# Performance work log

Measured on AMD Instinct MI355X. Metric: run time of the kernel, lower is better.

The kernel has to match this reference:

```python
import jax, jax.numpy as jnp
import numpy as np

ALPHA = 0.1
B, T, D = 32, 1024, 384


def _build_alive(T):
    # Expert j (1-indexed) is created at time j with lifetime 2^(ctz(j)+2)+1.
    def lifetime(j):
        k = (j & -j).bit_length() - 1
        return 2 ** (k + 2) + 1

    sets = [[j for j in range(1, t + 1) if t < j + lifetime(j)]
            for t in range(1, T + 1)]
    K = max(len(s) for s in sets)
    # pad with sentinel index T (the extra never-consumed expert slot)
    idx = np.full((T, K), T, dtype=np.int32)
    mask = np.zeros((T, K), dtype=np.float32)
    for t0, s in enumerate(sets):
        for i, j in enumerate(s):
            idx[t0, i] = j - 1  # 0-indexed expert slot
            mask[t0, i] = 1.0
    return idx, mask


def setup_inputs() -> dict:
    key = jax.random.key(0)
    kx, kw, kb = jax.random.split(key, 3)
    n_exp = T + 1
    x = jax.random.normal(kx, (B, T, D), dtype=jnp.float32)
    # stand-in STULayer = Linear(D, D) per expert
    W = jax.random.normal(kw, (n_exp, D, D), dtype=jnp.float32) / np.float32(np.sqrt(D))
    b = jax.random.normal(kb, (n_exp, D), dtype=jnp.float32) * 0.02
    idx, mask = _build_alive(T)
    return {"x": x, "W": W, "b": b,
            "alive_idx": jnp.asarray(idx), "alive_mask": jnp.asarray(mask)}


def reference(x, W, b, alive_idx, alive_mask):
    Bb, Tt, Dd = x.shape
    n_exp = W.shape[0]
    # initial pool: 1 expert with weight 1
    p0 = jnp.zeros((n_exp,), x.dtype).at[0].set(1.0)
    new_idx = jnp.arange(1, Tt + 1, dtype=jnp.int32)      # slot of expert created at step t
    t_f = jnp.arange(1, Tt + 1, dtype=x.dtype)            # p[new] = 1/t

    def step(p, inp):
        x_t, idx, mask, ni, tf = inp          # x_t: [B,D]; idx,mask: [K]
        Wg = W[idx]                            # [K,D,D]
        bg = b[idx]                            # [K,D]
        outs = jnp.einsum('bd,kde->kbe', x_t, Wg) + bg[:, None, :]  # [K,B,D]
        p_a = p[idx] * mask                    # weights of alive experts
        w = p_a / jnp.sum(p_a)                 # normalized (torch keeps them pre-normalized)
        y_t = jnp.einsum('k,kbe->be', w, outs)
        # soft cross-entropy of expert outputs against x_t (ChunkedCrossEntropyLoss stand-in)
        tgt = jax.nn.softmax(x_t, axis=-1)                       # [B,D]
        logp = jax.nn.log_softmax(outs, axis=-1)                 # [K,B,D]
        loss = -jnp.mean(jnp.sum(tgt[None, :, :] * logp, axis=-1), axis=-1)  # [K]
        loss = jax.lax.stop_gradient(loss)     # torch uses .item() => detached
        # multiplicative weight update, normalize over alive set
        p_upd = p_a * jnp.exp(-ALPHA * loss) * mask
        p_upd = p_upd / jnp.sum(p_upd)
        p = p.at[idx].set(jnp.where(mask > 0, p_upd, p[idx]))
        # spawn new expert with weight 1/t (renormalization deferred to use time)
        p = p.at[ni].set(1.0 / tf)
        return p, y_t

    xs = (jnp.swapaxes(x, 0, 1), alive_idx, alive_mask, new_idx, t_f)
    _, ys = jax.lax.scan(step, p0, xs)        # ys: [T,B,D]
    return jnp.swapaxes(ys, 0, 1)
```

## Files before the change

kernel.cpp:

```cpp
#include <hip/hip_runtime.h>

#define TT 1024
#define BB 32
#define DD 384
#define NE 1025
#define ALPHA_ 0.1f
#define TC 4
#define KSTEP 64
#define NKS 6
#define MROWS 128
#define PADK 72
#define NTHR 512

typedef __attribute__((ext_vector_type(8))) short short8;
typedef __attribute__((ext_vector_type(8))) unsigned short ushort8;
typedef __attribute__((ext_vector_type(4))) float f32x4;

__device__ __forceinline__ unsigned short f2bf(float f) {
    unsigned int u = __float_as_uint(f);
    unsigned int r = u + 0x7fffu + ((u >> 16) & 1u);
    return (unsigned short)(r >> 16);
}

__device__ __host__ __forceinline__ int chunks_of(int j, int* Lout) {
    int k = __builtin_ctz(j);
    int life = (1 << (k + 2)) + 1;
    int jend = j + life - 1; if (jend > TT) jend = TT;
    int L = jend - j + 1;
    *Lout = L;
    return (L + TC - 1) / TC;
}

__device__ __forceinline__ void gl16(const void* g, void* l) {
    __builtin_amdgcn_global_load_lds(
        (const __attribute__((address_space(1))) void*)g,
        (__attribute__((address_space(3))) void*)l, 16, 0, 0);
}

__device__ __forceinline__ float dppsum32(float v) {
    float t;
    t = __int_as_float(__builtin_amdgcn_update_dpp(0, __float_as_int(v), 0x111, 0xf, 0xf, true)); v += t;
    t = __int_as_float(__builtin_amdgcn_update_dpp(0, __float_as_int(v), 0x112, 0xf, 0xf, true)); v += t;
    t = __int_as_float(__builtin_amdgcn_update_dpp(0, __float_as_int(v), 0x114, 0xf, 0xf, true)); v += t;
    t = __int_as_float(__builtin_amdgcn_update_dpp(0, __float_as_int(v), 0x118, 0xf, 0xf, true)); v += t;
    t = __int_as_float(__builtin_amdgcn_update_dpp(0, __float_as_int(v), 0x142, 0xf, 0xf, true)); v += t;
    return __int_as_float(__builtin_amdgcn_readlane(__float_as_int(v), 31));
}

__global__ void setup_all(int* __restrict__ table, int* __restrict__ pref,
                          short* __restrict__ perm16,
                          const int* __restrict__ aidx, const float* __restrict__ amask,
                          int K) {
    __shared__ int sc[1024];
    int b = blockIdx.x, t = threadIdx.x;
    if (b == 0) {
        int j = t + 1;
        int L; int nc = chunks_of(j, &L);
        int start = 0;
        for (int jp = 1; jp < j; ++jp) { int Lp; start += chunks_of(jp, &Lp); }
        for (int c = 0; c < nc; ++c) {
            int cnt = L - c * TC; if (cnt > TC) cnt = TC;
            int* e = table + 3 * (start + c);
            e[0] = j - 1;
            e[1] = (j - 1) + c * TC;
            e[2] = cnt;
        }
    } else if (b == 1) {
        int c = 0;
        for (int kk = 0; kk < K; ++kk) c += (amask[t * K + kk] > 0.f) ? 1 : 0;
        sc[t] = c;
        __syncthreads();
        for (int off = 1; off < 1024; off <<= 1) {
            int v = (t >= off) ? sc[t - off] : 0;
            __syncthreads();
            sc[t] += v;
            __syncthreads();
        }
        if (t == 0) pref[0] = 0;
        pref[t + 1] = sc[t];
    } else {
        int t0 = b - 2;
        int l = t;
        if (l < 32) {
            short enc = 63;
            if (t0 >= 1 && t0 <= TT - 1 && l < K && amask[t0 * K + l] > 0.f) {
                int sp = aidx[t0 * K + l];
                if (sp == t0) enc = (short)(-sp);
                else {
                    for (int kk = 0; kk < K; ++kk)
                        if (aidx[(t0 - 1) * K + kk] == sp) { enc = (short)kk; break; }
                }
            }
            perm16[t0 * 32 + l] = enc;
        }
    }
}

__global__ __launch_bounds__(512)
void conv_w2(const float* __restrict__ W, unsigned short* __restrict__ Wperm) {
    int db = blockIdx.x;
    int j  = blockIdx.y;
    int tid = threadIdx.x, l = tid & 63, w8 = tid >> 6;
    const float* Wj = W + (size_t)j * (DD * DD)
                        + (size_t)(db * 32 + (l >> 4) * 8) * DD + (l & 15);
#pragma unroll
    for (int it = 0; it < 3; ++it) {
        int eblk = it * 8 + w8;
        const float* src = Wj + eblk * 16;
        ushort8 h;
#pragma unroll
        for (int k = 0; k < 8; ++k) h[k] = f2bf(src[(size_t)k * DD]);
        *(ushort8*)&Wperm[(((size_t)j * 12 + db) * 24 + eblk) * 512 + l * 8] = h;
    }
}

__global__ __launch_bounds__(512)
void conv_xt(const float* __restrict__ x, unsigned short* __restrict__ xperm,
             unsigned short* __restrict__ tgtbf) {
    int bidx = blockIdx.x;
    int tid = threadIdx.x;
    if (bidx < TT) {
        int t = bidx;
        int l = tid & 63, w8 = tid >> 6;
#pragma unroll
        for (int it = 0; it < 3; ++it) {
            int T = it * 8 + w8;
            int bb = T / 12, db = T - bb * 12;
            const float* src = x + ((size_t)(bb * 16 + (l & 15)) * TT + t) * DD
                                 + db * 32 + (l >> 4) * 8;
            float4 f0 = *(const float4*)src;
            float4 f1 = *(const float4*)(src + 4);
            ushort8 h;
            h[0] = f2bf(f0.x); h[1] = f2bf(f0.y); h[2] = f2bf(f0.z); h[3] = f2bf(f0.w);
            h[4] = f2bf(f1.x); h[5] = f2bf(f1.y); h[6] = f2bf(f1.z); h[7] = f2bf(f1.w);
            *(ushort8*)&xperm[(size_t)t * 12288 + T * 512 + l * 8] = h;
        }
    } else {
        __shared__ unsigned short sL[8 * 384];
        int blk = bidx - TT;
        int wid = tid >> 6, lane = tid & 63;
        size_t row = (size_t)blk * 8 + wid;
        const float* xr = x + row * DD;
        float v[6]; float m = -1e30f;
#pragma unroll
        for (int i = 0; i < 6; ++i) { v[i] = xr[lane + 64 * i]; m = fmaxf(m, v[i]); }
#pragma unroll
        for (int d = 1; d < 64; d <<= 1) m = fmaxf(m, __shfl_xor(m, d));
        float s = 0.f;
#pragma unroll
        for (int i = 0; i < 6; ++i) { v[i] = __expf(v[i] - m); s += v[i]; }
#pragma unroll
        for (int d = 1; d < 64; d <<= 1) s += __shfl_xor(s, d);
        float rz = 1.0f / s;
#pragma unroll
        for (int i = 0; i < 6; ++i) sL[wid * 384 + lane + 64 * i] = f2bf(v[i] * rz);
        __syncthreads();
        unsigned int* dst = (unsigned int*)(tgtbf + (size_t)blk * 8 * 384);
        const unsigned int* s32 = (const unsigned int*)sL;
#pragma unroll
        for (int i = 0; i < 3; ++i) dst[i * 512 + tid] = s32[i * 512 + tid];
    }
}

__global__ void conv_tgt(const float* __restrict__ x, unsigned short* __restrict__ tgtbf) {
    __shared__ unsigned short sL[8 * 384];
    int tid = threadIdx.x;
    int wid = tid >> 6, lane = tid & 63;
    size_t row = (size_t)blockIdx.x * 8 + wid;
    const float* xr = x + row * DD;
    float v[6]; float m = -1e30f;
#pragma unroll
    for (int i = 0; i < 6; ++i) { v[i] = xr[lane + 64 * i]; m = fmaxf(m, v[i]); }
#pragma unroll
    for (int d = 1; d < 64; d <<= 1) m = fmaxf(m, __shfl_xor(m, d));
    float s = 0.f;
#pragma unroll
    for (int i = 0; i < 6; ++i) { v[i] = __expf(v[i] - m); s += v[i]; }
#pragma unroll
    for (int d = 1; d < 64; d <<= 1) s += __shfl_xor(s, d);
    float rz = 1.0f / s;
#pragma unroll
    for (int i = 0; i < 6; ++i) sL[wid * 384 + lane + 64 * i] = f2bf(v[i] * rz);
    __syncthreads();
    unsigned int* dst = (unsigned int*)(tgtbf + (size_t)blockIdx.x * 8 * 384);
    const unsigned int* s32 = (const unsigned int*)sL;
#pragma unroll
    for (int i = 0; i < 3; ++i) dst[i * 512 + tid] = s32[i * 512 + tid];
}

__global__ __launch_bounds__(1024)
void gemmA(const unsigned short* __restrict__ xperm,
           const unsigned short* __restrict__ Wperm,
           const float* __restrict__ bias,
           const int* __restrict__ aidx,
           const unsigned short* __restrict__ tgtbf,
           float* __restrict__ Epad,
           const int* __restrict__ table, int nblk, int K,
           const int* __restrict__ pref,
           unsigned short* __restrict__ outs)
{
    __shared__ __align__(16) unsigned short sA[3][4096];
    __shared__ __align__(16) unsigned short sB[3][12288];
    __shared__ float sRow[128];
    __shared__ int sKK[TC];
    __shared__ int sSlot[TC];

    int bid = blockIdx.x;
    int q8 = nblk >> 3, r8 = nblk & 7;
    int xcd = bid & 7, pos = bid >> 3;
    int lb = (xcd < r8 ? xcd * (q8 + 1) : r8 * (q8 + 1) + (xcd - r8) * q8) + pos;

    int s = table[3 * lb], t0s = table[3 * lb + 1], cnt = table[3 * lb + 2];

    int tid = threadIdx.x;
    int wid = tid >> 6, lane = tid & 63;
    int waveM = wid >> 2, waveN = wid & 3;
    int lc = lane & 15, lg = lane >> 4;

    int tcl[4];
#pragma unroll
    for (int tc = 0; tc < 4; ++tc) { int t = t0s + tc; tcl[tc] = t > TT - 1 ? TT - 1 : t; }

    if (tid < TC) {
        int kk = 0, slot = 0;
        if (tid < cnt) {
            int t = t0s + tid;
            for (int k2 = 0; k2 < K; ++k2)
                if (aidx[t * K + k2] == s) { kk = k2; break; }
            if (pref) slot = pref[t] + kk;
        }
        sKK[tid] = kk;
        sSlot[tid] = slot;
    }

    f32x4 acc[2][6];
    f32x4 zz = {0.f, 0.f, 0.f, 0.f};
#pragma unroll
    for (int m = 0; m < 2; ++m)
#pragma unroll
        for (int n = 0; n < 6; ++n) acc[m][n] = zz;

    const size_t wbase = (size_t)s * (12 * 24 * 512);

    auto stage = [&](int buf, int ks) {
        if (wid < 8) {
            int tc = wid >> 1, bb = wid & 1;
            const unsigned short* asrc = xperm + ((size_t)tcl[tc] * 24 + bb * 12 + ks) * 512 + lane * 8;
            gl16(asrc, &sA[buf][wid * 512]);
            const unsigned short* bsrc = Wperm + wbase + ((size_t)ks * 24 + 16 + wid) * 512 + lane * 8;
            gl16(bsrc, &sB[buf][(16 + wid) * 512]);
        } else {
            int e0 = (wid - 8) * 2;
            const unsigned short* b0 = Wperm + wbase + ((size_t)ks * 24 + e0) * 512 + lane * 8;
            gl16(b0, &sB[buf][e0 * 512]);
            gl16(b0 + 512, &sB[buf][(e0 + 1) * 512]);
        }
    };

    stage(0, 0);
    stage(1, 1);
#pragma unroll
    for (int ks = 0; ks < 12; ++ks) {
        const int cur = ks % 3;
        if (ks < 11) asm volatile("s_waitcnt vmcnt(2)" ::: "memory");
        else         asm volatile("s_waitcnt vmcnt(0)" ::: "memory");
        __builtin_amdgcn_s_barrier();
        __builtin_amdgcn_sched_barrier(0);
        short8 af[2], bfr[6];
#pragma unroll
        for (int mf = 0; mf < 2; ++mf)
            af[mf] = *(const short8*)&sA[cur][(waveM * 2 + mf) * 512 + lane * 8];
#pragma unroll
        for (int nf = 0; nf < 6; ++nf)
            bfr[nf] = *(const short8*)&sB[cur][(waveN * 6 + nf) * 512 + lane * 8];
        __builtin_amdgcn_s_setprio(1);
#pragma unroll
        for (int mf = 0; mf < 2; ++mf)
#pragma unroll
            for (int nf = 0; nf < 6; ++nf)
                acc[mf][nf] = __builtin_amdgcn_mfma_f32_16x16x32_bf16(af[mf], bfr[nf], acc[mf][nf], 0, 0, 0);
        __builtin_amdgcn_s_setprio(0);
        __builtin_amdgcn_sched_barrier(0);
        if (ks < 10) stage((ks + 2) % 3, ks + 2);
    }
    __syncthreads();

    float* sStat = (float*)&sA[0][0];
#pragma unroll
    for (int nf = 0; nf < 6; ++nf) {
        float be = bias[(size_t)s * DD + waveN * 96 + nf * 16 + lc];
#pragma unroll
        for (int mf = 0; mf < 2; ++mf)
#pragma unroll
            for (int rr = 0; rr < 4; ++rr) acc[mf][nf][rr] += be;
    }
    if (outs && waveM < cnt) {
        unsigned short* ob = outs + (size_t)sSlot[waveM] * 12288;
#pragma unroll
        for (int mf = 0; mf < 2; ++mf)
#pragma unroll
            for (int nf = 0; nf < 6; ++nf) {
                int c2 = mf * 24 + waveN * 6 + nf;
                unsigned int lo, hi;
                asm("v_cvt_pk_bf16_f32 %0, %1, %2" : "=v"(lo)
                    : "v"(acc[mf][nf][0]), "v"(acc[mf][nf][1]));
                asm("v_cvt_pk_bf16_f32 %0, %1, %2" : "=v"(hi)
                    : "v"(acc[mf][nf][2]), "v"(acc[mf][nf][3]));
                uint2 pk; pk.x = lo; pk.y = hi;
                *(uint2*)&ob[c2 * 256 + lane * 4] = pk;
            }
    }
#pragma unroll
    for (int mf = 0; mf < 2; ++mf)
#pragma unroll
        for (int rr = 0; rr < 4; ++rr) {
            int row = waveM * 32 + mf * 16 + lg * 4 + rr;
            int tcr = row >> 5, b = row & 31;
            int t = tcl[tcr];
            const unsigned short* tg = tgtbf + ((size_t)b * TT + t) * DD;
            float psum = 0.f, pdot = 0.f;
#pragma unroll
            for (int nf = 0; nf < 6; ++nf) {
                int e = waveN * 96 + nf * 16 + lc;
                float a = acc[mf][nf][rr];
                psum += __expf(a);
                float tv = __uint_as_float(((unsigned int)tg[e]) << 16);
                pdot += tv * a;
            }
#pragma unroll
            for (int d = 1; d < 16; d <<= 1) { psum += __shfl_xor(psum, d); pdot += __shfl_xor(pdot, d); }
            if (lc == 0) { sStat[row * 12 + waveN] = psum; sStat[row * 12 + 4 + waveN] = pdot; }
        }
    __syncthreads();
    if (wid == 0) {
#pragma unroll
        for (int h = 0; h < 2; ++h) {
            int row = lane + h * 64;
            const f32x4 pp = *(const f32x4*)&sStat[row * 12];
            const f32x4 dd = *(const f32x4*)&sStat[row * 12 + 4];
            float S = pp[0] + pp[1] + pp[2] + pp[3];
            float Dt = dd[0] + dd[1] + dd[2] + dd[3];
            sRow[row] = __logf(S) - Dt;
        }
    }
    __syncthreads();
    if (wid == 0) {
#pragma unroll
        for (int pph = 0; pph < 2; ++pph) {
            int tc = pph * 2 + (lane >> 5);
            int b = lane & 31;
            float v = (tc < cnt) ? sRow[tc * 32 + b] : 0.f;
#pragma unroll
            for (int d = 1; d < 32; d <<= 1) v += __shfl_xor(v, d);
            if (b == 0 && tc < cnt) {
                float loss = v * (1.0f / 32.0f);
                float E = __expf(-ALPHA_ * loss);
                int t0 = t0s + tc;
                Epad[t0 * 32 + sKK[tc]] = E;
            }
        }
    }
}

__global__ __launch_bounds__(256)
void recur3(const float* __restrict__ Epad, const short* __restrict__ perm16,
            const int* __restrict__ aidx, const float* __restrict__ amask,
            float* __restrict__ wraw, int K) {
    __shared__ __align__(16) float sE[2][4096];
    __shared__ __align__(16) short sP[2][4160];
    int tid = threadIdx.x, wid = tid >> 6, lane = tid & 63;
    int l = lane;

    auto stageCh = [&](int buf, int c) {
        const float* eb = Epad + c * 4096;
#pragma unroll
        for (int i = wid; i < 16; i += 4)
            gl16(eb + i * 256 + lane * 4, &sE[buf][i * 256]);
        const short* pb = perm16 + (c * 128 + 1) * 32;
#pragma unroll
        for (int i = wid; i < 8; i += 4)
            gl16(pb + i * 512 + lane * 8, &sP[buf][32 + i * 512]);
    };

    stageCh(0, 0);
    __syncthreads();

    float pr = 0.f;
    if (l < K && amask[l] > 0.f && aidx[l] == 0) pr = 1.f;

    int buf = 0;
    for (int c = 0; c < 8; ++c) {
        if (c < 7) stageCh(buf ^ 1, c + 1);
        if (wid == 0) {
            float curE = (l < 32) ? sE[buf][l] : 0.f;
            short curP = (l < 32) ? sP[buf][32 + l] : (short)63;
            for (int tl = 0; tl < 128; ++tl) {
                float nE = 0.f; short nP = 63;
                if (tl < 127) {
                    nE = sE[buf][(tl + 1) * 32 + (l & 31)];
                    nP = sP[buf][(tl + 2) * 32 + (l & 31)];
                }
                int t = c * 128 + tl;
                if (l < 32) wraw[t * 32 + l] = pr;
                float qv = pr * curE;
                float S2 = dppsum32(qv);
                float pn = qv / S2;
                int pe = (l < 32) ? (int)curP : 63;
                int src = pe >= 0 ? pe : 0;
                float sv = __shfl(pn, src);
                pr = (pe >= 0) ? sv : (1.0f / (float)(-pe));
                curE = (l < 32) ? nE : 0.f;
                curP = nP;
            }
        }
        __syncthreads();
        buf ^= 1;
    }
}

__global__ void wnorm(float* __restrict__ w) {
    int tid = threadIdx.x;
    int wid = tid >> 6, lane = tid & 63;
    int half = lane >> 5, l = lane & 31;
    int t = blockIdx.x * 8 + wid * 2 + half;
    float v = w[t * 32 + l];
    float s = v;
#pragma unroll
    for (int d = 1; d < 32; d <<= 1) s += __shfl_xor(s, d);
    w[t * 32 + l] = v / s;
}

__global__ __launch_bounds__(512)
void mixout(const unsigned short* __restrict__ outs, const float* __restrict__ wraw,
            const int* __restrict__ pref, float* __restrict__ y) {
    int t = blockIdx.x;
    __shared__ float sW[32];
    int tid = threadIdx.x;
    if (tid < 32) {
        float v = wraw[t * 32 + tid];
        float s = v;
#pragma unroll
        for (int d = 1; d < 32; d <<= 1) s += __shfl_xor(s, d);
        sW[tid] = v / s;
    }
    __syncthreads();
    int p0 = pref[t];
    int L = pref[t + 1] - p0;
    float acc[24];
#pragma unroll
    for (int i = 0; i < 24; ++i) acc[i] = 0.f;
    const ushort8* base = (const ushort8*)(outs + (size_t)p0 * 12288);
    for (int kk = 0; kk < L; ++kk) {
        float w = sW[kk];
        const ushort8* sp = base + (size_t)kk * 1536;
#pragma unroll
        for (int pass = 0; pass < 3; ++pass) {
            ushort8 v = sp[pass * 512 + tid];
#pragma unroll
            for (int j = 0; j < 8; ++j)
                acc[pass * 8 + j] += w * __uint_as_float(((unsigned int)v[j]) << 16);
        }
    }
#pragma unroll
    for (int pass = 0; pass < 3; ++pass) {
        int idx = pass * 512 + tid;
        int c2 = idx >> 5;
        int lane0 = (idx * 2) & 63;
        int mf = (c2 >= 24) ? 1 : 0;
        int rem = c2 - mf * 24;
        int wN = rem / 6, nf = rem - wN * 6;
        int e0 = wN * 96 + nf * 16 + (lane0 & 15);
        int bb = mf * 16 + (lane0 >> 4) * 4;
#pragma unroll
        for (int r = 0; r < 4; ++r) {
            int b = bb + r;
            float2 st;
            st.x = acc[pass * 8 + r];
            st.y = acc[pass * 8 + 4 + r];
            *(float2*)&y[((size_t)b * TT + t) * DD + e0] = st;
        }
    }
}

__global__ void setup_blocks(int* __restrict__ table) {
    int j = threadIdx.x + 1;
    int L; int nc = chunks_of(j, &L);
    int start = 0;
    for (int jp = 1; jp < j; ++jp) { int Lp; start += chunks_of(jp, &Lp); }
    for (int c = 0; c < nc; ++c) {
        int cnt = L - c * TC; if (cnt > TC) cnt = TC;
        int* e = table + 3 * (start + c);
        e[0] = j - 1;
        e[1] = (j - 1) + c * TC;
        e[2] = cnt;
    }
}

__global__ void setup_union(int* __restrict__ uCount, int* __restrict__ uList) {
    int c = threadIdx.x;
    int t1 = 2 * c + 1, t2 = 2 * c + 2;
    int n = 0;
    for (int j = 1; j <= t2 && j <= TT; ++j) {
        int k = __builtin_ctz(j);
        int life = (1 << (k + 2)) + 1;
        if (j + life - 1 >= t1) { if (n < 32) uList[c * 32 + n] = j - 1; n++; }
    }
    uCount[c] = n > 32 ? 32 : n;
}

__global__ void setup_perm3(const int* __restrict__ aidx, const float* __restrict__ amask,
                            short* __restrict__ perm16, int K) {
    int t0 = blockIdx.x;
    int l = threadIdx.x;
    short enc = 63;
    if (t0 >= 1 && t0 <= TT - 1 && l < K && amask[t0 * K + l] > 0.f) {
        int sp = aidx[t0 * K + l];
        if (sp == t0) enc = (short)(-sp);
        else {
            for (int kk = 0; kk < K; ++kk)
                if (aidx[(t0 - 1) * K + kk] == sp) { enc = (short)kk; break; }
        }
    }
    perm16[t0 * 32 + l] = enc;
}

__global__ void conv_w(const float* __restrict__ W, unsigned short* __restrict__ Wperm) {
    int db = blockIdx.x;
    int j  = blockIdx.y;
    __shared__ __align__(16) unsigned short sL[12288];
    int tid = threadIdx.x;
    int r = tid >> 4, q = tid & 15;
    const float* src = W + (size_t)j * (DD * DD) + (size_t)(db * 32 + r) * DD + q * 24;
#pragma unroll
    for (int i = 0; i < 6; ++i) {
        float4 f = *(const float4*)(src + i * 4);
        int e0 = q * 24 + i * 4;
        float fv[4] = {f.x, f.y, f.z, f.w};
#pragma unroll
        for (int m = 0; m < 4; ++m) {
            int e = e0 + m;
            int off = (e >> 4) * 512 + (r >> 3) * 128 + (e & 15) * 8 + (r & 7);
            sL[off] = f2bf(fv[m]);
        }
    }
    __syncthreads();
    ushort8* dst = (ushort8*)(Wperm + ((size_t)j * 12 + db) * 12288);
    const ushort8* s8 = (const ushort8*)sL;
#pragma unroll
    for (int i = 0; i < 3; ++i) dst[tid * 3 + i] = s8[tid * 3 + i];
}

__global__ void conv_x(const float* __restrict__ x, unsigned short* __restrict__ xperm) {
    int t = blockIdx.x;
    __shared__ __align__(16) unsigned short sL[12288];
    int tid = threadIdx.x;
    int b = tid >> 4, q = tid & 15;
    const float* src = x + ((size_t)b * TT + t) * DD + q * 24;
#pragma unroll
    for (int i = 0; i < 6; ++i) {
        float4 f = *(const float4*)(src + i * 4);
        int d0 = q * 24 + i * 4;
        float fv[4] = {f.x, f.y, f.z, f.w};
#pragma unroll
        for (int m = 0; m < 4; ++m) {
            int d = d0 + m;
            int off = ((b >> 4) * 12 + (d >> 5)) * 512 + ((d >> 3) & 3) * 128 + (b & 15) * 8 + (d & 7);
            sL[off] = f2bf(fv[m]);
        }
    }
    __syncthreads();
    ushort8* dst = (ushort8*)(xperm + (size_t)t * 12288);
    const ushort8* s8 = (const ushort8*)sL;
#pragma unroll
    for (int i = 0; i < 3; ++i) dst[tid * 3 + i] = s8[tid * 3 + i];
}

__global__ __launch_bounds__(1024)
void gemmC(const unsigned short* __restrict__ xperm,
           const unsigned short* __restrict__ Wperm,
           const float* __restrict__ bias,
           const int* __restrict__ aidx,
           const float* __restrict__ wts32,
           const int* __restrict__ uCount, const int* __restrict__ uList,
           float* __restrict__ y, int K)
{
    __shared__ __align__(16) unsigned short sAF[24576];
    __shared__ __align__(16) unsigned short sB[2][12288];
    __shared__ float sWu[64];
    __shared__ int   sUL[32];
    __shared__ float sBv[768];

    int nb = gridDim.x;
    int bid = blockIdx.x;
    int q8 = nb >> 3, r8 = nb & 7;
    int xcd = bid & 7, pos = bid >> 3;
    int c = (xcd < r8 ? xcd * (q8 + 1) : r8 * (q8 + 1) + (xcd - r8) * q8) + pos;

    int t0 = c * 2;
    int tid = threadIdx.x, wid = tid >> 6, lane = tid & 63;
    int waveM = wid >> 2, waveN = wid & 3;
    int lc = lane & 15, lg = lane >> 4;
    int tcw = waveM >> 1, bbw = waveM & 1;

    int uc = uCount[c];
    if (tid < uc) sUL[tid] = uList[c * 32 + tid];
#pragma unroll
    for (int i = 0; i < 3; ++i) {
        int T = wid * 3 + i;
        int tc = T / 24, bb = (T / 12) & 1, db = T % 12;
        const unsigned short* src = xperm + ((size_t)(t0 + tc) * 24 + bb * 12 + db) * 512 + lane * 8;
        gl16(src, &sAF[T * 512]);
    }
    __syncthreads();
    if (tid < 2 * uc) {
        int u = tid >> 1, tc = tid & 1;
        int j = sUL[u];
        float wv = 0.f;
        for (int kk = 0; kk < K; ++kk)
            if (aidx[(t0 + tc) * K + kk] == j) { wv = wts32[(t0 + tc) * 32 + kk]; break; }
        sWu[u * 2 + tc] = wv;
    }
    __syncthreads();
    {
        size_t wb = (size_t)sUL[0] * (12 * 24 * 512);
        const unsigned short* b0 = Wperm + wb + (size_t)wid * 512 + lane * 8;
        gl16(b0, &sB[0][wid * 512]);
        if (wid < 8) {
            const unsigned short* b1 = Wperm + wb + (size_t)(16 + wid) * 512 + lane * 8;
            gl16(b1, &sB[0][(16 + wid) * 512]);
        }
    }
    for (int i = tid; i < 768; i += 1024) {
        int tc = (i >= 384) ? 1 : 0; int e = i - tc * 384;
        float a = 0.f;
        for (int u = 0; u < uc; ++u) a += sWu[u * 2 + tc] * bias[(size_t)sUL[u] * DD + e];
        sBv[i] = a;
    }
    __syncthreads();

    f32x4 accY[6], accE[6];
    f32x4 zz = {0.f, 0.f, 0.f, 0.f};
#pragma unroll
    for (int n = 0; n < 6; ++n) { accY[n] = zz; accE[n] = zz; }

    int buf = 0;
    for (int u = 0; u < uc; ++u) {
        float wv = sWu[u * 2 + tcw];
        bool act = (wv != 0.f);
        for (int ks = 0; ks < 12; ++ks) {
            int nu = u, nk = ks + 1;
            if (nk == 12) { nk = 0; nu = u + 1; }
            if (nu < uc) {
                size_t wb = (size_t)sUL[nu] * (12 * 24 * 512) + (size_t)nk * (24 * 512);
                const unsigned short* b0 = Wperm + wb + (size_t)wid * 512 + lane * 8;
                gl16(b0, &sB[buf ^ 1][wid * 512]);
                if (wid < 8) {
                    const unsigned short* b1 = Wperm + wb + (size_t)(16 + wid) * 512 + lane * 8;
                    gl16(b1, &sB[buf ^ 1][(16 + wid) * 512]);
                }
            }
            if (act) {
                short8 af = *(const short8*)&sAF[(waveM * 12 + ks) * 512 + lane * 8];
#pragma unroll
                for (int nf = 0; nf < 6; ++nf) {
                    short8 bf = *(const short8*)&sB[buf][(waveN * 6 + nf) * 512 + lane * 8];
                    accE[nf] = __builtin_amdgcn_mfma_f32_16x16x32_bf16(af, bf, accE[nf], 0, 0, 0);
                }
            }
            __syncthreads();
            buf ^= 1;
        }
        if (act) {
#pragma unroll
            for (int nf = 0; nf < 6; ++nf)
#pragma unroll
                for (int rr = 0; rr < 4; ++rr) { accY[nf][rr] += wv * accE[nf][rr]; accE[nf][rr] = 0.f; }
        }
    }

    int t = t0 + tcw;
#pragma unroll
    for (int nf = 0; nf < 6; ++nf) {
        int e = waveN * 96 + nf * 16 + lc;
        float bvv = sBv[tcw * 384 + e];
#pragma unroll
        for (int rr = 0; rr < 4; ++rr) {
            int b = bbw * 16 + lg * 4 + rr;
            y[((size_t)b * TT + t) * DD + e] = accY[nf][rr] + bvv;
        }
    }
}

__global__ void rowstats(const float* __restrict__ x, float* __restrict__ xm,
                         float* __restrict__ rz) {
    int wid = threadIdx.x >> 6;
    int lane = threadIdx.x & 63;
    int row = blockIdx.x * 4 + wid;
    const float* xr = x + (size_t)row * DD;
    float v[6];
    float m = -1e30f;
#pragma unroll
    for (int i = 0; i < 6; ++i) { v[i] = xr[lane + 64 * i]; m = fmaxf(m, v[i]); }
#pragma unroll
    for (int d = 1; d < 64; d <<= 1) m = fmaxf(m, __shfl_xor(m, d));
    float s = 0.f;
#pragma unroll
    for (int i = 0; i < 6; ++i) s += expf(v[i] - m);
#pragma unroll
    for (int d = 1; d < 64; d <<= 1) s += __shfl_xor(s, d);
    if (lane == 0) { xm[row] = m; rz[row] = 1.0f / s; }
}

template<int MODE>
__global__ __launch_bounds__(NTHR)
void gemm_phase(const float* __restrict__ x, const float* __restrict__ W,
                const float* __restrict__ bias, const int* __restrict__ aidx,
                const float* __restrict__ xm, const float* __restrict__ rz,
                const float* __restrict__ wts, float* __restrict__ Earr,
                float* __restrict__ y, const int* __restrict__ table,
                int nblk, int K)
{
    __shared__ __align__(16) unsigned short sA[MROWS * PADK];
    __shared__ __align__(16) unsigned short sB[DD * PADK];
    __shared__ float sRow[MROWS];
    __shared__ float sCoef[TC];

    int bid = blockIdx.x;
    int q = nblk >> 3, r = nblk & 7;
    int xcd = bid & 7, pos = bid >> 3;
    int lb = (xcd < r ? xcd * (q + 1) : r * (q + 1) + (xcd - r) * q) + pos;

    int s = table[3 * lb], t0s = table[3 * lb + 1], cnt = table[3 * lb + 2];

    int tid = threadIdx.x;
    int wid = tid >> 6, lane = tid & 63;
    int waveM = wid >> 2, waveN = wid & 3;
    int lc = lane & 15, lg = lane >> 4;

    if (MODE == 1 && tid < TC) {
        float c = 0.f;
        if (tid < cnt) {
            int t0 = t0s + tid;
            for (int kk = 0; kk < K; ++kk)
                if (aidx[t0 * K + kk] == s) { c = wts[t0 * K + kk]; break; }
        }
        sCoef[tid] = c;
    }

    f32x4 acc[4][6];
    f32x4 zz = {0.f, 0.f, 0.f, 0.f};
#pragma unroll
    for (int i = 0; i < 4; ++i)
#pragma unroll
        for (int n = 0; n < 6; ++n) acc[i][n] = zz;

    const float* Wj = W + (size_t)s * (DD * DD);

    int xr = tid >> 2, xq = tid & 3;
    int xtc = xr >> 5, xb = xr & 31;
    int xt = t0s + xtc; if (xt > TT - 1) xt = TT - 1;
    const float* xrow = x + ((size_t)xb * TT + xt) * DD;

    for (int ks = 0; ks < NKS; ++ks) {
        const int d0 = ks * KSTEP;
        __syncthreads();
        {
            const float4* src = (const float4*)(xrow + d0 + xq * 16);
            float4 f0 = src[0], f1 = src[1], f2 = src[2], f3 = src[3];
            short8 v0, v1;
            v0[0] = (short)f2bf(f0.x); v0[1] = (short)f2bf(f0.y);
            v0[2] = (short)f2bf(f0.z); v0[3] = (short)f2bf(f0.w);
            v0[4] = (short)f2bf(f1.x); v0[5] = (short)f2bf(f1.y);
            v0[6] = (short)f2bf(f1.z); v0[7] = (short)f2bf(f1.w);
            v1[0] = (short)f2bf(f2.x); v1[1] = (short)f2bf(f2.y);
            v1[2] = (short)f2bf(f2.z); v1[3] = (short)f2bf(f2.w);
            v1[4] = (short)f2bf(f3.x); v1[5] = (short)f2bf(f3.y);
            v1[6] = (short)f2bf(f3.z); v1[7] = (short)f2bf(f3.w);
            short8* dst = (short8*)&sA[xr * PADK + xq * 16];
            dst[0] = v0; dst[1] = v1;
        }
        {
            int dbase = d0 + wid * 8;
#pragma unroll
            for (int g = 0; g < 6; ++g) {
                int e = g * 64 + lane;
                const float* col = Wj + (size_t)dbase * DD + e;
                short8 h;
#pragma unroll
                for (int dd = 0; dd < 8; ++dd) h[dd] = (short)f2bf(col[(size_t)dd * DD]);
                *(short8*)&sB[e * PADK + wid * 8] = h;
            }
        }
        __syncthreads();
#pragma unroll
        for (int kh = 0; kh < 2; ++kh) {
            short8 af[4], bfr[6];
#pragma unroll
            for (int mf = 0; mf < 4; ++mf)
                af[mf] = *(const short8*)&sA[(waveM * 64 + mf * 16 + lc) * PADK + kh * 32 + lg * 8];
#pragma unroll
            for (int nf = 0; nf < 6; ++nf)
                bfr[nf] = *(const short8*)&sB[(waveN * 96 + nf * 16 + lc) * PADK + kh * 32 + lg * 8];
#pragma unroll
            for (int mf = 0; mf < 4; ++mf)
#pragma unroll
                for (int nf = 0; nf < 6; ++nf)
                    acc[mf][nf] = __builtin_amdgcn_mfma_f32_16x16x32_bf16(af[mf], bfr[nf], acc[mf][nf], 0, 0, 0);
        }
    }

    if (MODE == 0) {
        __syncthreads();
        float* sStat = (float*)sA;
#pragma unroll
        for (int nf = 0; nf < 6; ++nf) {
            float be = bias[(size_t)s * DD + waveN * 96 + nf * 16 + lc];
#pragma unroll
            for (int mf = 0; mf < 4; ++mf)
#pragma unroll
                for (int rr = 0; rr < 4; ++rr) acc[mf][nf][rr] += be;
        }
#pragma unroll
        for (int mf = 0; mf < 4; ++mf)
#pragma unroll
            for (int rr = 0; rr < 4; ++rr) {
                float m = acc[mf][0][rr];
#pragma unroll
                for (int nf = 1; nf < 6; ++nf) m = fmaxf(m, acc[mf][nf][rr]);
#pragma unroll
                for (int d = 1; d < 16; d <<= 1) m = fmaxf(m, __shfl_xor(m, d));
                if (lc == 0) sStat[(waveM * 64 + mf * 16 + lg * 4 + rr) * 12 + waveN] = m;
            }
        __syncthreads();
#pragma unroll
        for (int mf = 0; mf < 4; ++mf)
#pragma unroll
            for (int rr = 0; rr < 4; ++rr) {
                int row = waveM * 64 + mf * 16 + lg * 4 + rr;
                const f32x4 pm = *(const f32x4*)&sStat[row * 12];
                float rmax = fmaxf(fmaxf(pm[0], pm[1]), fmaxf(pm[2], pm[3]));
                int tc = row >> 5, b = row & 31;
                int t = t0s + tc; if (t > TT - 1) t = TT - 1;
                float xmv = xm[b * TT + t];
                float rzv = rz[b * TT + t];
                const float* x2 = x + ((size_t)b * TT + t) * DD;
                float psum = 0.f, pdot = 0.f;
#pragma unroll
                for (int nf = 0; nf < 6; ++nf) {
                    int e = waveN * 96 + nf * 16 + lc;
                    float a = acc[mf][nf][rr];
                    psum += __expf(a - rmax);
                    float tg = __expf(x2[e] - xmv) * rzv;
                    pdot += tg * a;
                }
#pragma unroll
                for (int d = 1; d < 16; d <<= 1) {
                    psum += __shfl_xor(psum, d);
                    pdot += __shfl_xor(pdot, d);
                }
                if (lc == 0) { sStat[row * 12 + 4 + waveN] = psum; sStat[row * 12 + 8 + waveN] = pdot; }
            }
        __syncthreads();
        if (wid == 0) {
#pragma unroll
            for (int h = 0; h < 2; ++h) {
                int row = lane + h * 64;
                const f32x4 mm = *(const f32x4*)&sStat[row * 12];
                const f32x4 pp = *(const f32x4*)&sStat[row * 12 + 4];
                const f32x4 dd = *(const f32x4*)&sStat[row * 12 + 8];
                float rmax = fmaxf(fmaxf(mm[0], mm[1]), fmaxf(mm[2], mm[3]));
                float S = pp[0] + pp[1] + pp[2] + pp[3];
                float Dt = dd[0] + dd[1] + dd[2] + dd[3];
                sRow[row] = rmax + logf(S) - Dt;
            }
        }
        __syncthreads();
        if (wid == 0) {
#pragma unroll
            for (int pph = 0; pph < 2; ++pph) {
                int tc = pph * 2 + (lane >> 5);
                int b = lane & 31;
                float v = (tc < cnt) ? sRow[tc * 32 + b] : 0.f;
#pragma unroll
                for (int d = 1; d < 32; d <<= 1) v += __shfl_xor(v, d);
                if (b == 0 && tc < cnt) {
                    float loss = v * (1.0f / 32.0f);
                    float E = expf(-ALPHA_ * loss);
                    int t0 = t0s + tc;
                    for (int kk = 0; kk < K; ++kk)
                        if (aidx[t0 * K + kk] == s) { Earr[t0 * K + kk] = E; break; }
                }
            }
        }
    } else {
#pragma unroll
        for (int mf = 0; mf < 4; ++mf)
#pragma unroll
            for (int rr = 0; rr < 4; ++rr) {
                int row = waveM * 64 + mf * 16 + lg * 4 + rr;
                int tc = row >> 5, b = row & 31;
                if (tc < cnt) {
                    float c = sCoef[tc];
                    int t = t0s + tc;
                    float* yr = y + ((size_t)b * TT + t) * DD + waveN * 96 + lc;
#pragma unroll
                    for (int nf = 0; nf < 6; ++nf)
                        atomicAdd(yr + nf * 16, c * acc[mf][nf][rr]);
                }
            }
    }
}

__global__ void recurrence(const int* __restrict__ aidx, const float* __restrict__ amask,
                           const float* __restrict__ Earr, float* __restrict__ wts, int K) {
    __shared__ float p[NE];
    int l = threadIdx.x;
    for (int i = l; i < NE; i += 64) p[i] = 0.f;
    __syncthreads();
    if (l == 0) p[0] = 1.f;
    __syncthreads();

    int idxv = TT; float mv = 0.f, Ev = 1.f;
    if (l < K) { idxv = aidx[l]; mv = amask[l]; Ev = Earr[l]; }

    for (int t0 = 0; t0 < TT; ++t0) {
        int idxn = TT; float mn = 0.f, En = 1.f;
        if (t0 + 1 < TT && l < K) {
            idxn = aidx[(t0 + 1) * K + l];
            mn = amask[(t0 + 1) * K + l];
            En = Earr[(t0 + 1) * K + l];
        }
        float pa = (l < K) ? p[idxv] * mv : 0.f;
        float qv = pa * Ev;
        float S1 = pa, S2 = qv;
#pragma unroll
        for (int d = 1; d < 64; d <<= 1) {
            S1 += __shfl_xor(S1, d);
            S2 += __shfl_xor(S2, d);
        }
        float w = pa / S1;
        if (l < K) wts[t0 * K + l] = w;
        float pn = qv / S2;
        __syncthreads();
        if (l < K && mv > 0.f) p[idxv] = pn;
        if (l == 0) p[t0 + 1] = 1.0f / (float)(t0 + 1);
        __syncthreads();
        idxv = idxn; mv = mn; Ev = En;
    }
}

__global__ void bias_init(const float* __restrict__ bias, const int* __restrict__ aidx,
                          const float* __restrict__ wts, float* __restrict__ y, int K) {
    int t0 = blockIdx.x;
    int e = threadIdx.x;
    float acc = 0.f;
    for (int kk = 0; kk < K; ++kk) {
        float w = wts[t0 * K + kk];
        int s = aidx[t0 * K + kk];
        acc += w * bias[(size_t)s * DD + e];
    }
    for (int b = 0; b < BB; ++b)
        y[((size_t)b * TT + t0) * DD + e] = acc;
}

extern "C" void kernel_launch(void* const* d_in, const int* in_sizes, int n_in,
                              void* d_out, int out_size, void* d_ws, size_t ws_size,
                              hipStream_t stream) {
    const float* x = (const float*)d_in[0];
    const float* W = (const float*)d_in[1];
    const float* bv = (const float*)d_in[2];
    const int* aidx = (const int*)d_in[3];
    const float* amask = (const float*)d_in[4];
    float* y = (float*)d_out;
    const int K = in_sizes[3] / TT;

    int nblk = 0, NSLOT = 0;
    for (int j = 1; j <= TT; ++j) { int L; nblk += chunks_of(j, &L); NSLOT += L; }

    size_t szW = (size_t)1024 * 294912;
    size_t szX = (size_t)1024 * 24576;
    size_t szT = (size_t)BB * TT * DD * 2;
    size_t szEp = (size_t)TT * 32 * sizeof(float);
    size_t szWt = (size_t)TT * 32 * sizeof(float);
    size_t szPm = (size_t)(TT + 1) * 32 * sizeof(short);
    size_t szTab = (size_t)6144 * 3 * sizeof(int);
    size_t szUC = 512 * sizeof(int);
    size_t szUL = 512 * 32 * sizeof(int);
    size_t szO  = (size_t)NSLOT * 12288 * 2;
    size_t szPf = (size_t)(TT + 1) * sizeof(int);
    size_t need2 = szW + szX + szT + szEp + szWt + szPm + szTab + szUC + szUL + 256;
    size_t need1 = need2 + szO + szPf;

    if (ws_size >= need1) {
        unsigned char* p = (unsigned char*)d_ws;
        unsigned short* Wperm = (unsigned short*)p; p += szW;
        unsigned short* xperm = (unsigned short*)p; p += szX;
        unsigned short* tgtb  = (unsigned short*)p; p += szT;
        float* Epad = (float*)p; p += szEp;
        float* wts32 = (float*)p; p += szWt;
        short* perm16 = (short*)p; p += szPm;
        int* table  = (int*)p;   p += szTab;
        int* uCnt   = (int*)p;   p += szUC;
        int* uLst   = (int*)p;   p += szUL;
        int* pref   = (int*)p;   p += szPf;
        unsigned short* outs = (unsigned short*)p; p += szO;

        hipLaunchKernelGGL(setup_all, dim3(TT + 3), dim3(1024), 0, stream,
                           table, pref, perm16, aidx, amask, K);
        hipLaunchKernelGGL(conv_w2, dim3(12, 1024), dim3(512), 0, stream, W, Wperm);
        hipLaunchKernelGGL(conv_xt, dim3(TT + BB * TT / 8), dim3(512), 0, stream,
                           x, xperm, tgtb);
        hipMemsetAsync(Epad, 0, szEp, stream);
        hipLaunchKernelGGL(gemmA, dim3(nblk), dim3(1024), 0, stream,
                           xperm, Wperm, bv, aidx, tgtb, Epad, table, nblk, K, pref, outs);
        hipLaunchKernelGGL(recur3, dim3(1), dim3(256), 0, stream,
                           Epad, perm16, aidx, amask, wts32, K);
        hipLaunchKernelGGL(mixout, dim3(TT), dim3(512), 0, stream, outs, wts32, pref, y);
    } else if (ws_size >= need2) {
        unsigned char* p = (unsigned char*)d_ws;
        unsigned short* Wperm = (unsigned short*)p; p += szW;
        unsigned short* xperm = (unsigned short*)p; p += szX;
        unsigned short* tgtb  = (unsigned short*)p; p += szT;
        float* Epad = (float*)p; p += szEp;
        float* wts32 = (float*)p; p += szWt;
        short* perm16 = (short*)p; p += szPm;
        int* table  = (int*)p;   p += szTab;
        int* uCnt   = (int*)p;   p += szUC;
        int* uLst   = (int*)p;   p += szUL;

        hipLaunchKernelGGL(setup_blocks, dim3(1), dim3(1024), 0, stream, table);
        hipLaunchKernelGGL(setup_union, dim3(1), dim3(512), 0, stream, uCnt, uLst);
        hipLaunchKernelGGL(setup_perm3, dim3(TT + 1), dim3(32), 0, stream, aidx, amask, perm16, K);
        hipLaunchKernelGGL(conv_w, dim3(12, 1024), dim3(512), 0, stream, W, Wperm);
        hipLaunchKernelGGL(conv_x, dim3(TT), dim3(512), 0, stream, x, xperm);
        hipLaunchKernelGGL(conv_tgt, dim3(BB * TT / 8), dim3(512), 0, stream, x, tgtb);
        hipMemsetAsync(Epad, 0, szEp, stream);
        hipLaunchKernelGGL(gemmA, dim3(nblk), dim3(1024), 0, stream,
                           xperm, Wperm, bv, aidx, tgtb, Epad, table, nblk, K,
                           (const int*)nullptr, (unsigned short*)nullptr);
        hipLaunchKernelGGL(recur3, dim3(1), dim3(256), 0, stream,
                           Epad, perm16, aidx, amask, wts32, K);
        hipLaunchKernelGGL(wnorm, dim3(TT / 8), dim3(256), 0, stream, wts32);
        hipLaunchKernelGGL(gemmC, dim3(512), dim3(1024), 0, stream,
                           xperm, Wperm, bv, aidx, wts32, uCnt, uLst, y, K);
    } else {
        float* Earr = (float*)d_ws;
        float* wts = Earr + (size_t)TT * K;
        float* xm = wts + (size_t)TT * K;
        float* rz = xm + (size_t)BB * TT;
        int* table = (int*)(rz + (size_t)BB * TT);

        hipLaunchKernelGGL(setup_blocks, dim3(1), dim3(1024), 0, stream, table);
        hipLaunchKernelGGL(rowstats, dim3(BB * TT / 4), dim3(256), 0, stream, x, xm, rz);
        hipLaunchKernelGGL((gemm_phase<0>), dim3(nblk), dim3(NTHR), 0, stream,
                           x, W, bv, aidx, xm, rz, (const float*)nullptr, Earr,
                           (float*)nullptr, table, nblk, K);
        hipLaunchKernelGGL(recurrence, dim3(1), dim3(64), 0, stream, aidx, amask, Earr, wts, K);
        hipLaunchKernelGGL(bias_init, dim3(TT), dim3(DD), 0, stream, bv, aidx, wts, y, K);
        hipLaunchKernelGGL((gemm_phase<1>), dim3(nblk), dim3(NTHR), 0, stream,
                           x, W, bv, aidx, xm, rz, wts, (float*)nullptr, y, table, nblk, K);
    }
}
```

Before: 965.3 us.

## Load GEMM fragments directly from global memory, dropping LDS staging pipeline

Replaces the triple-buffered LDS staging of x and W tiles (async global-to-LDS loads plus per-step barriers) with direct per-wave global loads of MFMA fragments into registers. This removes the LDS footprint and synchronisation cost and may allow more resident blocks. In exchange, each W fragment is fetched by all four row-waves separately, multiplying cache traffic, and load latency is no longer overlapped by explicit prefetch.

```diff
diff --git a/kernel.cpp b/kernel.cpp
--- a/kernel.cpp
+++ b/kernel.cpp
@@ -199,8 +199,7 @@
            const int* __restrict__ pref,
            unsigned short* __restrict__ outs)
 {
-    __shared__ __align__(16) unsigned short sA[3][4096];
-    __shared__ __align__(16) unsigned short sB[3][12288];
+    __shared__ float sStat[128 * 12];
     __shared__ float sRow[128];
     __shared__ int sKK[TC];
     __shared__ int sSlot[TC];
@@ -217,9 +216,7 @@
     int waveM = wid >> 2, waveN = wid & 3;
     int lc = lane & 15, lg = lane >> 4;
 
-    int tcl[4];
-#pragma unroll
-    for (int tc = 0; tc < 4; ++tc) { int t = t0s + tc; tcl[tc] = t > TT - 1 ? TT - 1 : t; }
+    int tW = t0s + waveM; if (tW > TT - 1) tW = TT - 1;
 
     if (tid < TC) {
         int kk = 0, slot = 0;
@@ -240,52 +237,28 @@
 #pragma unroll
         for (int n = 0; n < 6; ++n) acc[m][n] = zz;
 
-    const size_t wbase = (size_t)s * (12 * 24 * 512);
-
-    auto stage = [&](int buf, int ks) {
-        if (wid < 8) {
-            int tc = wid >> 1, bb = wid & 1;
-            const unsigned short* asrc = xperm + ((size_t)tcl[tc] * 24 + bb * 12 + ks) * 512 + lane * 8;
-            gl16(asrc, &sA[buf][wid * 512]);
-            const unsigned short* bsrc = Wperm + wbase + ((size_t)ks * 24 + 16 + wid) * 512 + lane * 8;
-            gl16(bsrc, &sB[buf][(16 + wid) * 512]);
-        } else {
-            int e0 = (wid - 8) * 2;
-            const unsigned short* b0 = Wperm + wbase + ((size_t)ks * 24 + e0) * 512 + lane * 8;
-            gl16(b0, &sB[buf][e0 * 512]);
-            gl16(b0 + 512, &sB[buf][(e0 + 1) * 512]);
-        }
-    };
-
-    stage(0, 0);
-    stage(1, 1);
+    const unsigned short* aPtr = xperm + ((size_t)tW * 24) * 512 + lane * 8;
+    const unsigned short* bPtr = Wperm + (size_t)s * (12 * 24 * 512)
+                                       + (size_t)(waveN * 6) * 512 + lane * 8;
+
 #pragma unroll
     for (int ks = 0; ks < 12; ++ks) {
-        const int cur = ks % 3;
-        if (ks < 11) asm volatile("s_waitcnt vmcnt(2)" ::: "memory");
-        else         asm volatile("s_waitcnt vmcnt(0)" ::: "memory");
-        __builtin_amdgcn_s_barrier();
-        __builtin_amdgcn_sched_barrier(0);
-        short8 af[2], bfr[6];
-#pragma unroll
-        for (int mf = 0; mf < 2; ++mf)
-            af[mf] = *(const short8*)&sA[cur][(waveM * 2 + mf) * 512 + lane * 8];
+        short8 af0 = *(const short8*)(aPtr + (size_t)ks * 512);
+        short8 af1 = *(const short8*)(aPtr + (size_t)(12 + ks) * 512);
+        short8 bf[6];
 #pragma unroll
         for (int nf = 0; nf < 6; ++nf)
-            bfr[nf] = *(const short8*)&sB[cur][(waveN * 6 + nf) * 512 + lane * 8];
+            bf[nf] = *(const short8*)(bPtr + (size_t)ks * 12288 + nf * 512);
         __builtin_amdgcn_s_setprio(1);
 #pragma unroll
-        for (int mf = 0; mf < 2; ++mf)
-#pragma unroll
-            for (int nf = 0; nf < 6; ++nf)
-                acc[mf][nf] = __builtin_amdgcn_mfma_f32_16x16x32_bf16(af[mf], bfr[nf], acc[mf][nf], 0, 0, 0);
+        for (int nf = 0; nf < 6; ++nf) {
+            acc[0][nf] = __builtin_amdgcn_mfma_f32_16x16x32_bf16(af0, bf[nf], acc[0][nf], 0, 0, 0);
+            acc[1][nf] = __builtin_amdgcn_mfma_f32_16x16x32_bf16(af1, bf[nf], acc[1][nf], 0, 0, 0);
+        }
         __builtin_amdgcn_s_setprio(0);
-        __builtin_amdgcn_sched_barrier(0);
-        if (ks < 10) stage((ks + 2) % 3, ks + 2);
-    }
-    __syncthreads();
-
-    float* sStat = (float*)&sA[0][0];
+    }
+    __syncthreads();
+
 #pragma unroll
     for (int nf = 0; nf < 6; ++nf) {
         float be = bias[(size_t)s * DD + waveN * 96 + nf * 16 + lc];
@@ -315,9 +288,8 @@
 #pragma unroll
         for (int rr = 0; rr < 4; ++rr) {
             int row = waveM * 32 + mf * 16 + lg * 4 + rr;
-            int tcr = row >> 5, b = row & 31;
-            int t = tcl[tcr];
-            const unsigned short* tg = tgtbf + ((size_t)b * TT + t) * DD;
+            int b = row & 31;
+            const unsigned short* tg = tgtbf + ((size_t)b * TT + tW) * DD;
             float psum = 0.f, pdot = 0.f;
 #pragma unroll
             for (int nf = 0; nf < 6; ++nf) {
```

New measurement: 1.052 ms. 9.0% more time.
